# Optimization experiments

Measured on AMD Instinct MI355X. Metric: run time of the kernel, lower is better.

The kernel has to match this reference:

```python
import jax, jax.numpy as jnp
import numpy as np

N, E, F_IN, D, H = 20000, 640000, 128, 16, 8  # nodes, edges, in_features, out_features, n_heads


def _linear_params(k, fan_in, fan_out):
    W = jax.random.normal(k, (fan_in, fan_out), jnp.float32) / np.sqrt(fan_in)
    b = jnp.zeros((fan_out,), jnp.float32)
    return W, b


def setup_inputs() -> dict:
    key = jax.random.key(0)
    ks = jax.random.split(key, 8)
    x = jax.random.normal(ks[0], (N, F_IN), jnp.float32)
    edge_index = jax.random.randint(ks[1], (2, E), 0, N, dtype=jnp.int64)
    Wq, bq = _linear_params(ks[2], F_IN, D * H)
    Wk, bk = _linear_params(ks[3], F_IN, D * H)
    Wv, bv = _linear_params(ks[4], F_IN, D * H)
    Wpsi, bpsi = _linear_params(ks[5], D, D)
    Wo, bo = _linear_params(ks[6], D * H * 2, F_IN)
    gamma = jnp.ones((F_IN,), jnp.float32)
    beta = jnp.zeros((F_IN,), jnp.float32)
    return {"x": x, "edge_index": edge_index, "Wq": Wq, "bq": bq, "Wk": Wk, "bk": bk,
            "Wv": Wv, "bv": bv, "Wpsi": Wpsi, "bpsi": bpsi, "Wo": Wo, "bo": bo,
            "gamma": gamma, "beta": beta}


def _segment_softmax(logits, seg, num_segments):
    # numerically-stable softmax of edge logits grouped by destination node (row)
    m = jax.ops.segment_max(logits, seg, num_segments=num_segments)  # [N,H]
    m = jnp.where(jnp.isfinite(m), m, 0.0)
    e = jnp.exp(logits - m[seg])  # [E,H]
    s = jax.ops.segment_sum(e, seg, num_segments=num_segments)  # [N,H]
    return e / (s[seg] + 1e-16)


def reference(x, edge_index, Wq, bq, Wk, bk, Wv, bv, Wpsi, bpsi, Wo, bo, gamma, beta):
    q = (x @ Wq + bq).reshape(N, H, D)
    k = (x @ Wk + bk).reshape(N, H, D)
    v = (x @ Wv + bv).reshape(N, H, D)
    row, col = edge_index[0], edge_index[1]

    logits = jnp.einsum('ehd,ehd->eh', q[row], k[col]) / np.sqrt(D)  # [E,H]
    alpha = _segment_softmax(logits, row, N)  # [E,H]

    v_j = v[col]  # [E,H,D]
    h_lp = jax.ops.segment_sum((alpha[..., None] * v_j).reshape(E, H * D), row, num_segments=N)
    v_bp = jnp.tanh(v_j @ Wpsi + bpsi)  # per-head linear on last dim, [E,H,D]
    h_bp = jax.ops.segment_sum((alpha[..., None] * v_bp).reshape(E, H * D), row, num_segments=N)

    h_out = jnp.concatenate([h_lp, h_bp], axis=1) @ Wo + bo  # [N,F_IN]
    y = x + jax.nn.relu(h_out)
    mu = jnp.mean(y, axis=-1, keepdims=True)
    var = jnp.mean(jnp.square(y - mu), axis=-1, keepdims=True)
    return (y - mu) * jax.lax.rsqrt(var + 1e-5) * gamma + beta
```

## Files before the change

### kernel.cpp

```cpp
#include <hip/hip_runtime.h>
#include <hip/hip_bf16.h>
#include <math.h>

#define NN 20000
#define EE 640000
#define NCH 8
#define CHN 2500
#define SLOT 24

typedef __attribute__((ext_vector_type(8))) short short8;
typedef __attribute__((ext_vector_type(4))) float f32x4;
typedef __hip_bfloat16 bf16;
typedef __hip_bfloat162 bf162;

__device__ inline ushort f2bf(float f) {
  bf16 h = __float2bfloat16(f);
  return *(ushort*)&h;
}
__device__ inline float2 ldbf2(const ushort* p) {
  return __bfloat1622float2(*(const bf162*)p);
}
__device__ inline float2 bf2u(uint u) {
  return __bfloat1622float2(*(const bf162*)&u);
}
__device__ inline float fast_tanh(float x) {
  float xx = fminf(fmaxf(x, -9.0f), 9.0f);
  float e = exp2f(xx * 2.885390082f);
  return (e - 1.0f) * __builtin_amdgcn_rcpf(e + 1.0f);
}


__global__ __launch_bounds__(256) void qkv_mfma(
    const float* __restrict__ x,
    const float* __restrict__ Wq, const float* __restrict__ bq,
    const float* __restrict__ Wk, const float* __restrict__ bk,
    const float* __restrict__ Wv, const float* __restrict__ bv,
    const float* __restrict__ Wpsi, const float* __restrict__ bpsi,
    float* __restrict__ qbuf, ushort* __restrict__ kvb,
    int* __restrict__ cursor2) {
  __shared__ ushort As[128 * 136];
  __shared__ ushort Bts[128 * 136];
  __shared__ float Wps[256];
  __shared__ float bps[16];
  int t = threadIdx.x;
  {
    int flat = (blockIdx.y * 157 + blockIdx.x) * 256 + t;
    for (int j = flat; j < NN * NCH; j += 157 * 3 * 256) cursor2[j] = 0;
  }
  int n0 = blockIdx.x * 128;
  int mat = blockIdx.y;
  const float* W    = mat == 0 ? Wq : (mat == 1 ? Wk : Wv);
  const float* bias = mat == 0 ? bq : (mat == 1 ? bk : bv);
  if (mat == 2) {
    Wps[t] = Wpsi[t];
    if (t < 16) bps[t] = bpsi[t];
  }

  {
    int r = t >> 1, half = (t & 1) * 64;
    int n = n0 + r;
    ushort* dst = &As[r * 136 + half];
    if (n < NN) {
      const float* src = x + (size_t)n * 128 + half;
#pragma unroll
      for (int j = 0; j < 8; ++j) {
        float4 f0 = *(const float4*)(src + 8 * j);
        float4 f1 = *(const float4*)(src + 8 * j + 4);
        ushort tmp[8] = {f2bf(f0.x), f2bf(f0.y), f2bf(f0.z), f2bf(f0.w),
                         f2bf(f1.x), f2bf(f1.y), f2bf(f1.z), f2bf(f1.w)};
        *(uint4*)(dst + 8 * j) = *(uint4*)tmp;
      }
    } else {
#pragma unroll
      for (int j = 0; j < 8; ++j) *(uint4*)(dst + 8 * j) = make_uint4(0, 0, 0, 0);
    }
  }
  {
    int k = t >> 1, nh = (t & 1) * 64;
    const float* src = W + (size_t)k * 128 + nh;
#pragma unroll
    for (int i = 0; i < 16; ++i) {
      float4 f = *(const float4*)(src + 4 * i);
      Bts[(nh + 4 * i + 0) * 136 + k] = f2bf(f.x);
      Bts[(nh + 4 * i + 1) * 136 + k] = f2bf(f.y);
      Bts[(nh + 4 * i + 2) * 136 + k] = f2bf(f.z);
      Bts[(nh + 4 * i + 3) * 136 + k] = f2bf(f.w);
    }
  }
  __syncthreads();

  int w = t >> 6, lane = t & 63;
  int m = lane & 15, q = lane >> 4;
  int r0 = w * 32;
  f32x4 acc0[8], acc1[8];
#pragma unroll
  for (int c = 0; c < 8; ++c) {
    acc0[c] = (f32x4){0.f, 0.f, 0.f, 0.f};
    acc1[c] = (f32x4){0.f, 0.f, 0.f, 0.f};
  }
#pragma unroll
  for (int kb = 0; kb < 4; ++kb) {
    int kof = kb * 32 + 8 * q;
    short8 a0 = *(const short8*)&As[(r0 + m) * 136 + kof];
    short8 a1 = *(const short8*)&As[(r0 + 16 + m) * 136 + kof];
#pragma unroll
    for (int c = 0; c < 8; ++c) {
      short8 b = *(const short8*)&Bts[(c * 16 + m) * 136 + kof];
      acc0[c] = __builtin_amdgcn_mfma_f32_16x16x32_bf16(a0, b, acc0[c], 0, 0, 0);
      acc1[c] = __builtin_amdgcn_mfma_f32_16x16x32_bf16(a1, b, acc1[c], 0, 0, 0);
    }
  }
  if (mat == 2) __syncthreads();

  int koff2 = (mat == 2) ? 2 : 0;
#pragma unroll
  for (int c = 0; c < 8; ++c) {
    int col = c * 16 + m;
    float bb = bias[col];
    size_t pos = (size_t)(col >> 1) * 6 + (col & 1) + koff2;
#pragma unroll
    for (int reg = 0; reg < 4; ++reg) {
      int rl0 = r0 + 4 * q + reg;
      int rl1 = rl0 + 16;
      int row0 = n0 + rl0;
      int row1 = n0 + rl1;
      float v0 = acc0[c][reg] + bb;
      float v1 = acc1[c][reg] + bb;
      if (mat == 0) {
        if (row0 < NN) qbuf[(size_t)row0 * 128 + col] = v0;
        if (row1 < NN) qbuf[(size_t)row1 * 128 + col] = v1;
      } else {
        if (row0 < NN) kvb[(size_t)row0 * 384 + pos] = f2bf(v0);
        if (row1 < NN) kvb[(size_t)row1 * 384 + pos] = f2bf(v1);
        if (mat == 2) {
          Bts[rl0 * 136 + col] = f2bf(v0);
          Bts[rl1 * 136 + col] = f2bf(v1);
        }
      }
    }
  }

  if (mat == 2) {
    __syncthreads();
#pragma unroll
    for (int ii = 0; ii < 4; ++ii) {
      int idx = ii * 256 + t;
      int rloc = idx >> 3, h = idx & 7;
      int n = n0 + rloc;
      const ushort* vp = &Bts[rloc * 136 + h * 16];
      uint4 a = *(const uint4*)vp;
      uint4 b = *(const uint4*)(vp + 8);
      float v[16];
      {
        float2 f;
        f = bf2u(a.x); v[0] = f.x;  v[1] = f.y;
        f = bf2u(a.y); v[2] = f.x;  v[3] = f.y;
        f = bf2u(a.z); v[4] = f.x;  v[5] = f.y;
        f = bf2u(a.w); v[6] = f.x;  v[7] = f.y;
        f = bf2u(b.x); v[8] = f.x;  v[9] = f.y;
        f = bf2u(b.y); v[10] = f.x; v[11] = f.y;
        f = bf2u(b.z); v[12] = f.x; v[13] = f.y;
        f = bf2u(b.w); v[14] = f.x; v[15] = f.y;
      }
      float o[16];
#pragma unroll
      for (int d = 0; d < 16; ++d) o[d] = bps[d];
#pragma unroll
      for (int dp = 0; dp < 16; ++dp) {
        float vv = v[dp];
#pragma unroll
        for (int d = 0; d < 16; ++d) o[d] = fmaf(vv, Wps[dp * 16 + d], o[d]);
      }
      if (n < NN) {
        ushort* dst = kvb + (size_t)n * 384;
#pragma unroll
        for (int j = 0; j < 8; ++j) {
          uint u = (uint)f2bf(fast_tanh(o[2 * j])) |
                   ((uint)f2bf(fast_tanh(o[2 * j + 1])) << 16);
          *(uint*)(dst + (8 * h + j) * 6 + 4) = u;
        }
      }
    }
  }
}

__global__ __launch_bounds__(256) void scatter_kernel(
    const int* __restrict__ ei,
    int* __restrict__ cursor2, ushort* __restrict__ scol2) {
  int e = blockIdx.x * 256 + threadIdx.x;
  if (e < EE) {
    int r = ei[e];
    int c = ei[EE + e];
    int ch = c / CHN;
    int pos = atomicAdd(&cursor2[r * NCH + ch], 1);
    if (pos < SLOT) scol2[(r * NCH + ch) * SLOT + pos] = (ushort)c;
  }
}

__global__ __launch_bounds__(256) void aggregate_kernel(
    const float* __restrict__ qbuf, const ushort* __restrict__ kvb,
    const int* __restrict__ cursor2, const ushort* __restrict__ scol2,
    ushort* __restrict__ hbufb) {
  int t = threadIdx.x;
  int lane = t & 63;
  int wid = __builtin_amdgcn_readfirstlane(t >> 6);
  int wg = blockIdx.x * 4 + wid;
  int n0 = wg * 4;
  int h = lane >> 3, dg = (lane & 7) * 2;
  int off = h * 16 + dg;
  const float SC = 0.25f * 1.44269504f;

  float q2x[4], q2y[4], s[4], aV0[4], aV1[4], aB0[4], aB1[4];
#pragma unroll
  for (int ni = 0; ni < 4; ++ni) {
    float2 q2 = *(const float2*)(qbuf + (size_t)(n0 + ni) * 128 + off);
    q2x[ni] = q2.x * SC; q2y[ni] = q2.y * SC;
    s[ni] = 0.f; aV0[ni] = 0.f; aV1[ni] = 0.f; aB0[ni] = 0.f; aB1[ni] = 0.f;
  }
  int mycnt = cursor2[n0 * NCH + (lane & 31)];

  const char* kvc = (const char*)kvb;
  uint lo = (uint)lane * 12u;

  for (int ch = 0; ch < NCH; ++ch) {
#pragma unroll
    for (int ni = 0; ni < 4; ++ni) {
      int cnt = __builtin_amdgcn_readfirstlane(__shfl(mycnt, ni * NCH + ch));
      cnt = cnt > SLOT ? SLOT : cnt;
      if (cnt == 0) continue;
      const uint* slu = (const uint*)(scol2 + ((n0 + ni) * NCH + ch) * SLOT);
      float lq2x = q2x[ni], lq2y = q2y[ni];
      float ls = 0.f, lV0 = 0.f, lV1 = 0.f, lB0 = 0.f, lB1 = 0.f;

      struct U3 { uint x, y, z; };
      auto proc = [&](U3 u) {
        float2 kk = bf2u(u.x);
        float2 vv = bf2u(u.y);
        float2 tb = bf2u(u.z);
        float d = fmaf(lq2x, kk.x, lq2y * kk.y);
        d += __shfl_xor(d, 1);
        d += __shfl_xor(d, 2);
        d += __shfl_xor(d, 4);
        float wgt = exp2f(d);
        ls += wgt;
        lV0 = fmaf(wgt, vv.x, lV0); lV1 = fmaf(wgt, vv.y, lV1);
        lB0 = fmaf(wgt, tb.x, lB0); lB1 = fmaf(wgt, tb.y, lB1);
      };

      int i = 0;
      for (; i + 4 <= cnt; i += 4) {
        uint w0 = slu[i >> 1];
        uint w1 = slu[(i >> 1) + 1];
        uint e0 = w0 & 0xffffu, e1 = w0 >> 16, e2 = w1 & 0xffffu, e3 = w1 >> 16;
        const char* p0 = kvc + e0 * 768u;
        const char* p1 = kvc + e1 * 768u;
        const char* p2 = kvc + e2 * 768u;
        const char* p3 = kvc + e3 * 768u;
        U3 u0 = *(const U3*)(p0 + lo);
        U3 u1 = *(const U3*)(p1 + lo);
        U3 u2 = *(const U3*)(p2 + lo);
        U3 u3 = *(const U3*)(p3 + lo);
        proc(u0); proc(u1); proc(u2); proc(u3);
      }
      for (; i < cnt; ++i) {
        uint wv = slu[i >> 1];
        uint e = (i & 1) ? (wv >> 16) : (wv & 0xffffu);
        const char* p = kvc + e * 768u;
        U3 u = *(const U3*)(p + lo);
        proc(u);
      }
      s[ni] += ls;
      aV0[ni] += lV0; aV1[ni] += lV1; aB0[ni] += lB0; aB1[ni] += lB1;
    }
    __syncthreads();
  }

#pragma unroll
  for (int ni = 0; ni < 4; ++ni) {
    float inv = s[ni] > 0.f ? 1.f / s[ni] : 0.f;
    ushort* hp = hbufb + (size_t)(n0 + ni) * 256 + off;
    uint uv = (uint)f2bf(aV0[ni] * inv) | ((uint)f2bf(aV1[ni] * inv) << 16);
    uint ub = (uint)f2bf(aB0[ni] * inv) | ((uint)f2bf(aB1[ni] * inv) << 16);
    *(uint*)(hp)       = uv;
    *(uint*)(hp + 128) = ub;
  }
}

__global__ __launch_bounds__(256) void output_mfma(
    const ushort* __restrict__ hbufb, const float* __restrict__ x,
    const float* __restrict__ Wo, const float* __restrict__ bo,
    const float* __restrict__ gamma, const float* __restrict__ beta,
    float* __restrict__ out) {
  __shared__ ushort As[128 * 136];
  __shared__ ushort Bts[128 * 136];
  __shared__ float bos[128], gs[128], bts[128];
  int t = threadIdx.x;
  int n0 = blockIdx.x * 128;
  if (t < 128) { bos[t] = bo[t]; gs[t] = gamma[t]; bts[t] = beta[t]; }
  int w = t >> 6, lane = t & 63;
  int m = lane & 15, q = lane >> 4;
  int r0 = w * 32;
  f32x4 acc0[8], acc1[8];
#pragma unroll
  for (int c = 0; c < 8; ++c) {
    acc0[c] = (f32x4){0.f, 0.f, 0.f, 0.f};
    acc1[c] = (f32x4){0.f, 0.f, 0.f, 0.f};
  }
  for (int kc = 0; kc < 2; ++kc) {
    if (kc) __syncthreads();
    {
      int r = t >> 1, half = (t & 1) * 64;
      int n = n0 + r;
      ushort* dst = &As[r * 136 + half];
      if (n < NN) {
        const ushort* src = hbufb + (size_t)n * 256 + kc * 128 + half;
#pragma unroll
        for (int j = 0; j < 8; ++j)
          *(uint4*)(dst + 8 * j) = *(const uint4*)(src + 8 * j);
      } else {
#pragma unroll
        for (int j = 0; j < 8; ++j) *(uint4*)(dst + 8 * j) = make_uint4(0, 0, 0, 0);
      }
    }
    {
      int k = t >> 1, nh = (t & 1) * 64;
      const float* src = Wo + (size_t)(kc * 128 + k) * 128 + nh;
#pragma unroll
      for (int i = 0; i < 16; ++i) {
        float4 f = *(const float4*)(src + 4 * i);
        Bts[(nh + 4 * i + 0) * 136 + k] = f2bf(f.x);
        Bts[(nh + 4 * i + 1) * 136 + k] = f2bf(f.y);
        Bts[(nh + 4 * i + 2) * 136 + k] = f2bf(f.z);
        Bts[(nh + 4 * i + 3) * 136 + k] = f2bf(f.w);
      }
    }
    __syncthreads();
#pragma unroll
    for (int kb = 0; kb < 4; ++kb) {
      int kof = kb * 32 + 8 * q;
      short8 a0 = *(const short8*)&As[(r0 + m) * 136 + kof];
      short8 a1 = *(const short8*)&As[(r0 + 16 + m) * 136 + kof];
#pragma unroll
      for (int c = 0; c < 8; ++c) {
        short8 b = *(const short8*)&Bts[(c * 16 + m) * 136 + kof];
        acc0[c] = __builtin_amdgcn_mfma_f32_16x16x32_bf16(a0, b, acc0[c], 0, 0, 0);
        acc1[c] = __builtin_amdgcn_mfma_f32_16x16x32_bf16(a1, b, acc1[c], 0, 0, 0);
      }
    }
  }
#pragma unroll
  for (int half = 0; half < 2; ++half) {
#pragma unroll
    for (int reg = 0; reg < 4; ++reg) {
      int row = n0 + r0 + half * 16 + 4 * q + reg;
      bool valid = row < NN;
      float vals[8];
      float sum = 0.f;
#pragma unroll
      for (int c = 0; c < 8; ++c) {
        int col = c * 16 + m;
        float a = (half ? acc1[c][reg] : acc0[c][reg]) + bos[col];
        a = fmaxf(a, 0.f);
        float xv = valid ? x[(size_t)row * 128 + col] : 0.f;
        float v = a + xv;
        vals[c] = v;
        sum += v;
      }
      sum += __shfl_xor(sum, 1); sum += __shfl_xor(sum, 2);
      sum += __shfl_xor(sum, 4); sum += __shfl_xor(sum, 8);
      float mean = sum * (1.f / 128.f);
      float ssq = 0.f;
#pragma unroll
      for (int c = 0; c < 8; ++c) {
        float d = vals[c] - mean;
        ssq = fmaf(d, d, ssq);
      }
      ssq += __shfl_xor(ssq, 1); ssq += __shfl_xor(ssq, 2);
      ssq += __shfl_xor(ssq, 4); ssq += __shfl_xor(ssq, 8);
      float rstd = rsqrtf(ssq * (1.f / 128.f) + 1e-5f);
      if (valid) {
#pragma unroll
        for (int c = 0; c < 8; ++c) {
          int col = c * 16 + m;
          out[(size_t)row * 128 + col] = (vals[c] - mean) * rstd * gs[col] + bts[col];
        }
      }
    }
  }
}

extern "C" void kernel_launch(void* const* d_in, const int* in_sizes, int n_in,
                              void* d_out, int out_size, void* d_ws, size_t ws_size,
                              hipStream_t stream) {
  const float* x     = (const float*)d_in[0];
  const int*   ei    = (const int*)d_in[1];
  const float* Wq    = (const float*)d_in[2];
  const float* bq    = (const float*)d_in[3];
  const float* Wk    = (const float*)d_in[4];
  const float* bk    = (const float*)d_in[5];
  const float* Wv    = (const float*)d_in[6];
  const float* bv    = (const float*)d_in[7];
  const float* Wpsi  = (const float*)d_in[8];
  const float* bpsi  = (const float*)d_in[9];
  const float* Wo    = (const float*)d_in[10];
  const float* bo    = (const float*)d_in[11];
  const float* gamma = (const float*)d_in[12];
  const float* beta  = (const float*)d_in[13];
  float* out = (float*)d_out;

  char* ws = (char*)d_ws;
  float*  qbuf    = (float*) (ws);
  ushort* kvb     = (ushort*)(ws + 10240000);
  ushort* hbufb   = (ushort*)(ws + 25600000);
  int*    cursor2 = (int*)   (ws + 35840000);
  ushort* scol2   = (ushort*)(ws + 36480000);

  qkv_mfma<<<dim3(157, 3), 256, 0, stream>>>(x, Wq, bq, Wk, bk, Wv, bv,
                                             Wpsi, bpsi, qbuf, kvb, cursor2);
  scatter_kernel<<<2500, 256, 0, stream>>>(ei, cursor2, scol2);
  aggregate_kernel<<<1250, 256, 0, stream>>>(qbuf, kvb, cursor2, scol2, hbufb);
  output_mfma<<<157, 256, 0, stream>>>(hbufb, x, Wo, bo, gamma, beta, out);
}
```

Measured before the change: 227.3 us.

## Regroup K/V/tanh layout into 4-element chunks and process two edges per wave

```diff
diff --git a/kernel.cpp b/kernel.cpp
--- a/kernel.cpp
+++ b/kernel.cpp
@@ -112,12 +112,12 @@
   }
   if (mat == 2) __syncthreads();
 
-  int koff2 = (mat == 2) ? 2 : 0;
+  int koff2 = (mat == 2) ? 4 : 0;
 #pragma unroll
   for (int c = 0; c < 8; ++c) {
     int col = c * 16 + m;
     float bb = bias[col];
-    size_t pos = (size_t)(col >> 1) * 6 + (col & 1) + koff2;
+    size_t pos = (size_t)(c * 4 + (m >> 2)) * 12 + (m & 3) + koff2;
 #pragma unroll
     for (int reg = 0; reg < 4; ++reg) {
       int rl0 = r0 + 4 * q + reg;
@@ -177,7 +177,9 @@
         for (int j = 0; j < 8; ++j) {
           uint u = (uint)f2bf(fast_tanh(o[2 * j])) |
                    ((uint)f2bf(fast_tanh(o[2 * j + 1])) << 16);
-          *(uint*)(dst + (8 * h + j) * 6 + 4) = u;
+          int grp = h * 4 + (j >> 1);
+          int within = (2 * j) & 3;
+          *(uint*)(dst + grp * 12 + 8 + within) = u;
         }
       }
     }
@@ -205,84 +207,95 @@
   int lane = t & 63;
   int wid = __builtin_amdgcn_readfirstlane(t >> 6);
   int wg = blockIdx.x * 4 + wid;
-  int n0 = wg * 4;
-  int h = lane >> 3, dg = (lane & 7) * 2;
-  int off = h * 16 + dg;
+  int n0 = wg * 2;
+  int l31 = lane & 31;
+  int half = lane >> 5;
   const float SC = 0.25f * 1.44269504f;
 
-  float q2x[4], q2y[4], s[4], aV0[4], aV1[4], aB0[4], aB1[4];
-#pragma unroll
-  for (int ni = 0; ni < 4; ++ni) {
-    float2 q2 = *(const float2*)(qbuf + (size_t)(n0 + ni) * 128 + off);
-    q2x[ni] = q2.x * SC; q2y[ni] = q2.y * SC;
-    s[ni] = 0.f; aV0[ni] = 0.f; aV1[ni] = 0.f; aB0[ni] = 0.f; aB1[ni] = 0.f;
-  }
-  int mycnt = cursor2[n0 * NCH + (lane & 31)];
+  float4 q0 = *(const float4*)(qbuf + (size_t)n0 * 128 + l31 * 4);
+  float4 q1 = *(const float4*)(qbuf + (size_t)(n0 + 1) * 128 + l31 * 4);
+  q0.x *= SC; q0.y *= SC; q0.z *= SC; q0.w *= SC;
+  q1.x *= SC; q1.y *= SC; q1.z *= SC; q1.w *= SC;
+
+  int mycnt = cursor2[n0 * NCH + (lane & 15)];
+
+  float s0 = 0.f, s1 = 0.f;
+  float4 aV0 = make_float4(0.f, 0.f, 0.f, 0.f), aV1 = aV0;
+  float4 aB0 = aV0, aB1 = aV0;
 
   const char* kvc = (const char*)kvb;
-  uint lo = (uint)lane * 12u;
+  uint lo24 = (uint)l31 * 24u;
 
   for (int ch = 0; ch < NCH; ++ch) {
 #pragma unroll
-    for (int ni = 0; ni < 4; ++ni) {
+    for (int ni = 0; ni < 2; ++ni) {
       int cnt = __builtin_amdgcn_readfirstlane(__shfl(mycnt, ni * NCH + ch));
       cnt = cnt > SLOT ? SLOT : cnt;
       if (cnt == 0) continue;
       const uint* slu = (const uint*)(scol2 + ((n0 + ni) * NCH + ch) * SLOT);
-      float lq2x = q2x[ni], lq2y = q2y[ni];
-      float ls = 0.f, lV0 = 0.f, lV1 = 0.f, lB0 = 0.f, lB1 = 0.f;
-
-      struct U3 { uint x, y, z; };
-      auto proc = [&](U3 u) {
-        float2 kk = bf2u(u.x);
-        float2 vv = bf2u(u.y);
-        float2 tb = bf2u(u.z);
-        float d = fmaf(lq2x, kk.x, lq2y * kk.y);
+      float4 q = ni ? q1 : q0;
+      float ls = 0.f;
+      float4 lV = make_float4(0.f, 0.f, 0.f, 0.f);
+      float4 lB = make_float4(0.f, 0.f, 0.f, 0.f);
+      int npair = (cnt + 1) >> 1;
+      for (int p = 0; p < npair; ++p) {
+        uint wv = slu[p];
+        uint e0 = wv & 0xffffu;
+        uint e1 = wv >> 16;
+        bool pv = (2 * p + 1) < cnt;
+        uint e1c = pv ? e1 : e0;
+        uint e = half ? e1c : e0;
+        const char* pb = kvc + (size_t)e * 768u + lo24;
+        uint4 L0 = *(const uint4*)pb;
+        uint2 L1 = *(const uint2*)(pb + 16);
+        float2 k0 = bf2u(L0.x), k1 = bf2u(L0.y);
+        float d = fmaf(q.x, k0.x, fmaf(q.y, k0.y, fmaf(q.z, k1.x, q.w * k1.y)));
         d += __shfl_xor(d, 1);
         d += __shfl_xor(d, 2);
-        d += __shfl_xor(d, 4);
         float wgt = exp2f(d);
+        wgt = (half && !pv) ? 0.f : wgt;
         ls += wgt;
-        lV0 = fmaf(wgt, vv.x, lV0); lV1 = fmaf(wgt, vv.y, lV1);
-        lB0 = fmaf(wgt, tb.x, lB0); lB1 = fmaf(wgt, tb.y, lB1);
-      };
-
-      int i = 0;
-      for (; i + 4 <= cnt; i += 4) {
-        uint w0 = slu[i >> 1];
-        uint w1 = slu[(i >> 1) + 1];
-        uint e0 = w0 & 0xffffu, e1 = w0 >> 16, e2 = w1 & 0xffffu, e3 = w1 >> 16;
-        const char* p0 = kvc + e0 * 768u;
-        const char* p1 = kvc + e1 * 768u;
-        const char* p2 = kvc + e2 * 768u;
-        const char* p3 = kvc + e3 * 768u;
-        U3 u0 = *(const U3*)(p0 + lo);
-        U3 u1 = *(const U3*)(p1 + lo);
-        U3 u2 = *(const U3*)(p2 + lo);
-        U3 u3 = *(const U3*)(p3 + lo);
-        proc(u0); proc(u1); proc(u2); proc(u3);
-      }
-      for (; i < cnt; ++i) {
-        uint wv = slu[i >> 1];
-        uint e = (i & 1) ? (wv >> 16) : (wv & 0xffffu);
-        const char* p = kvc + e * 768u;
-        U3 u = *(const U3*)(p + lo);
-        proc(u);
-      }
-      s[ni] += ls;
-      aV0[ni] += lV0; aV1[ni] += lV1; aB0[ni] += lB0; aB1[ni] += lB1;
+        float2 v0 = bf2u(L0.z), v1 = bf2u(L0.w);
+        lV.x = fmaf(wgt, v0.x, lV.x); lV.y = fmaf(wgt, v0.y, lV.y);
+        lV.z = fmaf(wgt, v1.x, lV.z); lV.w = fmaf(wgt, v1.y, lV.w);
+        float2 b0 = bf2u(L1.x), b1 = bf2u(L1.y);
+        lB.x = fmaf(wgt, b0.x, lB.x); lB.y = fmaf(wgt, b0.y, lB.y);
+        lB.z = fmaf(wgt, b1.x, lB.z); lB.w = fmaf(wgt, b1.y, lB.w);
+      }
+      if (ni == 0) {
+        s0 += ls;
+        aV0.x += lV.x; aV0.y += lV.y; aV0.z += lV.z; aV0.w += lV.w;
+        aB0.x += lB.x; aB0.y += lB.y; aB0.z += lB.z; aB0.w += lB.w;
+      } else {
+        s1 += ls;
+        aV1.x += lV.x; aV1.y += lV.y; aV1.z += lV.z; aV1.w += lV.w;
+        aB1.x += lB.x; aB1.y += lB.y; aB1.z += lB.z; aB1.w += lB.w;
+      }
     }
     __syncthreads();
   }
 
 #pragma unroll
-  for (int ni = 0; ni < 4; ++ni) {
-    float inv = s[ni] > 0.f ? 1.f / s[ni] : 0.f;
-    ushort* hp = hbufb + (size_t)(n0 + ni) * 256 + off;
-    uint uv = (uint)f2bf(aV0[ni] * inv) | ((uint)f2bf(aV1[ni] * inv) << 16);
-    uint ub = (uint)f2bf(aB0[ni] * inv) | ((uint)f2bf(aB1[ni] * inv) << 16);
-    *(uint*)(hp)       = uv;
-    *(uint*)(hp + 128) = ub;
+  for (int ni = 0; ni < 2; ++ni) {
+    float s = ni ? s1 : s0;
+    float4 V = ni ? aV1 : aV0;
+    float4 B = ni ? aB1 : aB0;
+    s += __shfl_xor(s, 32);
+    V.x += __shfl_xor(V.x, 32); V.y += __shfl_xor(V.y, 32);
+    V.z += __shfl_xor(V.z, 32); V.w += __shfl_xor(V.w, 32);
+    B.x += __shfl_xor(B.x, 32); B.y += __shfl_xor(B.y, 32);
+    B.z += __shfl_xor(B.z, 32); B.w += __shfl_xor(B.w, 32);
+    float inv = s > 0.f ? 1.f / s : 0.f;
+    if (half == 0) {
+      ushort* hp = hbufb + (size_t)(n0 + ni) * 256 + l31 * 4;
+      uint2 uv, ub;
+      uv.x = (uint)f2bf(V.x * inv) | ((uint)f2bf(V.y * inv) << 16);
+      uv.y = (uint)f2bf(V.z * inv) | ((uint)f2bf(V.w * inv) << 16);
+      ub.x = (uint)f2bf(B.x * inv) | ((uint)f2bf(B.y * inv) << 16);
+      ub.y = (uint)f2bf(B.z * inv) | ((uint)f2bf(B.w * inv) << 16);
+      *(uint2*)(hp)       = uv;
+      *(uint2*)(hp + 128) = ub;
+    }
   }
 }
 
@@ -418,6 +431,6 @@
   qkv_mfma<<<dim3(157, 3), 256, 0, stream>>>(x, Wq, bq, Wk, bk, Wv, bv,
                                              Wpsi, bpsi, qbuf, kvb, cursor2);
   scatter_kernel<<<2500, 256, 0, stream>>>(ei, cursor2, scol2);
-  aggregate_kernel<<<1250, 256, 0, stream>>>(qbuf, kvb, cursor2, scol2, hbufb);
+  aggregate_kernel<<<2500, 256, 0, stream>>>(qbuf, kvb, cursor2, scol2, hbufb);
   output_mfma<<<157, 256, 0, stream>>>(hbufb, x, Wo, bo, gamma, beta, out);
 }
```

After: 233.8 us. 2.8% more time.

## Fuse edge scatter into QKV kernel and simplify aggregation to per-node CSR rows

Applied to the files above, without the earlier changes.

```diff
diff --git a/kernel.cpp b/kernel.cpp
--- a/kernel.cpp
+++ b/kernel.cpp
@@ -4,9 +4,6 @@
 
 #define NN 20000
 #define EE 640000
-#define NCH 8
-#define CHN 2500
-#define SLOT 24
 
 typedef __attribute__((ext_vector_type(8))) short short8;
 typedef __attribute__((ext_vector_type(4))) float f32x4;
@@ -16,9 +13,6 @@
 __device__ inline ushort f2bf(float f) {
   bf16 h = __float2bfloat16(f);
   return *(ushort*)&h;
-}
-__device__ inline float2 ldbf2(const ushort* p) {
-  return __bfloat1622float2(*(const bf162*)p);
 }
 __device__ inline float2 bf2u(uint u) {
   return __bfloat1622float2(*(const bf162*)&u);
@@ -36,19 +30,28 @@
     const float* __restrict__ Wk, const float* __restrict__ bk,
     const float* __restrict__ Wv, const float* __restrict__ bv,
     const float* __restrict__ Wpsi, const float* __restrict__ bpsi,
-    float* __restrict__ qbuf, ushort* __restrict__ kvb,
-    int* __restrict__ cursor2) {
+    const int* __restrict__ ei,
+    float* __restrict__ qbuf,
+    ushort* __restrict__ kb, ushort* __restrict__ vb2, ushort* __restrict__ bb2,
+    int* __restrict__ cursor, ushort* __restrict__ scol) {
   __shared__ ushort As[128 * 136];
-  __shared__ ushort Bts[128 * 136];
+  __shared__ ushort WB[128 * 136];
   __shared__ float Wps[256];
   __shared__ float bps[16];
   int t = threadIdx.x;
+  int mat = blockIdx.y;
+
   {
-    int flat = (blockIdx.y * 157 + blockIdx.x) * 256 + t;
-    for (int j = flat; j < NN * NCH; j += 157 * 3 * 256) cursor2[j] = 0;
-  }
+    int flat = (mat * 157 + blockIdx.x) * 256 + t;
+    for (int e = flat; e < EE; e += 157 * 3 * 256) {
+      int r = ei[e];
+      int c = ei[EE + e];
+      int pos = atomicAdd(&cursor[r], 1);
+      if (pos < 128) scol[r * 128 + pos] = (ushort)c;
+    }
+  }
+
   int n0 = blockIdx.x * 128;
-  int mat = blockIdx.y;
   const float* W    = mat == 0 ? Wq : (mat == 1 ? Wk : Wv);
   const float* bias = mat == 0 ? bq : (mat == 1 ? bk : bv);
   if (mat == 2) {
@@ -81,10 +84,10 @@
 #pragma unroll
     for (int i = 0; i < 16; ++i) {
       float4 f = *(const float4*)(src + 4 * i);
-      Bts[(nh + 4 * i + 0) * 136 + k] = f2bf(f.x);
-      Bts[(nh + 4 * i + 1) * 136 + k] = f2bf(f.y);
-      Bts[(nh + 4 * i + 2) * 136 + k] = f2bf(f.z);
-      Bts[(nh + 4 * i + 3) * 136 + k] = f2bf(f.w);
+      WB[(nh + 4 * i + 0) * 136 + k] = f2bf(f.x);
+      WB[(nh + 4 * i + 1) * 136 + k] = f2bf(f.y);
+      WB[(nh + 4 * i + 2) * 136 + k] = f2bf(f.z);
+      WB[(nh + 4 * i + 3) * 136 + k] = f2bf(f.w);
     }
   }
   __syncthreads();
@@ -99,55 +102,54 @@
     acc1[c] = (f32x4){0.f, 0.f, 0.f, 0.f};
   }
 #pragma unroll
-  for (int kb = 0; kb < 4; ++kb) {
-    int kof = kb * 32 + 8 * q;
+  for (int kb_ = 0; kb_ < 4; ++kb_) {
+    int kof = kb_ * 32 + 8 * q;
     short8 a0 = *(const short8*)&As[(r0 + m) * 136 + kof];
     short8 a1 = *(const short8*)&As[(r0 + 16 + m) * 136 + kof];
 #pragma unroll
     for (int c = 0; c < 8; ++c) {
-      short8 b = *(const short8*)&Bts[(c * 16 + m) * 136 + kof];
+      short8 b = *(const short8*)&WB[(c * 16 + m) * 136 + kof];
       acc0[c] = __builtin_amdgcn_mfma_f32_16x16x32_bf16(a0, b, acc0[c], 0, 0, 0);
       acc1[c] = __builtin_amdgcn_mfma_f32_16x16x32_bf16(a1, b, acc1[c], 0, 0, 0);
     }
   }
-  if (mat == 2) __syncthreads();
-
-  int koff2 = (mat == 2) ? 2 : 0;
+
+  if (mat == 0) {
+#pragma unroll
+    for (int c = 0; c < 8; ++c) {
+      int col = c * 16 + m;
+      float bb = bias[col];
+#pragma unroll
+      for (int reg = 0; reg < 4; ++reg) {
+        int row0 = n0 + r0 + 4 * q + reg;
+        int row1 = row0 + 16;
+        if (row0 < NN) qbuf[(size_t)row0 * 128 + col] = acc0[c][reg] + bb;
+        if (row1 < NN) qbuf[(size_t)row1 * 128 + col] = acc1[c][reg] + bb;
+      }
+    }
+    return;
+  }
+
+  __syncthreads();
 #pragma unroll
   for (int c = 0; c < 8; ++c) {
     int col = c * 16 + m;
     float bb = bias[col];
-    size_t pos = (size_t)(col >> 1) * 6 + (col & 1) + koff2;
 #pragma unroll
     for (int reg = 0; reg < 4; ++reg) {
       int rl0 = r0 + 4 * q + reg;
-      int rl1 = rl0 + 16;
-      int row0 = n0 + rl0;
-      int row1 = n0 + rl1;
-      float v0 = acc0[c][reg] + bb;
-      float v1 = acc1[c][reg] + bb;
-      if (mat == 0) {
-        if (row0 < NN) qbuf[(size_t)row0 * 128 + col] = v0;
-        if (row1 < NN) qbuf[(size_t)row1 * 128 + col] = v1;
-      } else {
-        if (row0 < NN) kvb[(size_t)row0 * 384 + pos] = f2bf(v0);
-        if (row1 < NN) kvb[(size_t)row1 * 384 + pos] = f2bf(v1);
-        if (mat == 2) {
-          Bts[rl0 * 136 + col] = f2bf(v0);
-          Bts[rl1 * 136 + col] = f2bf(v1);
-        }
-      }
-    }
-  }
+      As[rl0 * 136 + col]        = f2bf(acc0[c][reg] + bb);
+      As[(rl0 + 16) * 136 + col] = f2bf(acc1[c][reg] + bb);
+    }
+  }
+  __syncthreads();
 
   if (mat == 2) {
-    __syncthreads();
 #pragma unroll
     for (int ii = 0; ii < 4; ++ii) {
-      int idx = ii * 256 + t;
-      int rloc = idx >> 3, h = idx & 7;
-      int n = n0 + rloc;
-      const ushort* vp = &Bts[rloc * 136 + h * 16];
+      int cell = ii * 256 + t;
+      int rl = cell >> 3, h = cell & 7;
+      const ushort* vp = &As[rl * 136 + h * 16];
       uint4 a = *(const uint4*)vp;
       uint4 b = *(const uint4*)(vp + 8);
       float v[16];
@@ -171,119 +173,100 @@
 #pragma unroll
         for (int d = 0; d < 16; ++d) o[d] = fmaf(vv, Wps[dp * 16 + d], o[d]);
       }
-      if (n < NN) {
-        ushort* dst = kvb + (size_t)n * 384;
-#pragma unroll
-        for (int j = 0; j < 8; ++j) {
-          uint u = (uint)f2bf(fast_tanh(o[2 * j])) |
-                   ((uint)f2bf(fast_tanh(o[2 * j + 1])) << 16);
-          *(uint*)(dst + (8 * h + j) * 6 + 4) = u;
-        }
-      }
-    }
-  }
-}
-
-__global__ __launch_bounds__(256) void scatter_kernel(
-    const int* __restrict__ ei,
-    int* __restrict__ cursor2, ushort* __restrict__ scol2) {
-  int e = blockIdx.x * 256 + threadIdx.x;
-  if (e < EE) {
-    int r = ei[e];
-    int c = ei[EE + e];
-    int ch = c / CHN;
-    int pos = atomicAdd(&cursor2[r * NCH + ch], 1);
-    if (pos < SLOT) scol2[(r * NCH + ch) * SLOT + pos] = (ushort)c;
+      ushort* dst = &WB[rl * 136 + h * 16];
+#pragma unroll
+      for (int j = 0; j < 8; ++j) {
+        uint u = (uint)f2bf(fast_tanh(o[2 * j])) |
+                 ((uint)f2bf(fast_tanh(o[2 * j + 1])) << 16);
+        *(uint*)(dst + 2 * j) = u;
+      }
+    }
+    __syncthreads();
+  }
+
+  {
+    int r = t >> 1, hh = (t & 1) * 64;
+    int n = n0 + r;
+    if (n < NN) {
+      ushort* dstA = (mat == 1 ? kb : vb2) + (size_t)n * 128 + hh;
+      const ushort* srcA = &As[r * 136 + hh];
+#pragma unroll
+      for (int j = 0; j < 8; ++j)
+        *(uint4*)(dstA + 8 * j) = *(const uint4*)(srcA + 8 * j);
+      if (mat == 2) {
+        ushort* dstB = bb2 + (size_t)n * 128 + hh;
+        const ushort* srcB = &WB[r * 136 + hh];
+#pragma unroll
+        for (int j = 0; j < 8; ++j)
+          *(uint4*)(dstB + 8 * j) = *(const uint4*)(srcB + 8 * j);
+      }
+    }
   }
 }
 
 __global__ __launch_bounds__(256) void aggregate_kernel(
-    const float* __restrict__ qbuf, const ushort* __restrict__ kvb,
-    const int* __restrict__ cursor2, const ushort* __restrict__ scol2,
+    const float* __restrict__ qbuf,
+    const ushort* __restrict__ kb, const ushort* __restrict__ vb2,
+    const ushort* __restrict__ bb2,
+    const int* __restrict__ cursor, const ushort* __restrict__ scol,
     ushort* __restrict__ hbufb) {
-  int t = threadIdx.x;
-  int lane = t & 63;
-  int wid = __builtin_amdgcn_readfirstlane(t >> 6);
-  int wg = blockIdx.x * 4 + wid;
-  int n0 = wg * 4;
+  int wid = threadIdx.x >> 6, lane = threadIdx.x & 63;
+  int node = blockIdx.x * 4 + wid;
   int h = lane >> 3, dg = (lane & 7) * 2;
   int off = h * 16 + dg;
   const float SC = 0.25f * 1.44269504f;
-
-  float q2x[4], q2y[4], s[4], aV0[4], aV1[4], aB0[4], aB1[4];
-#pragma unroll
-  for (int ni = 0; ni < 4; ++ni) {
-    float2 q2 = *(const float2*)(qbuf + (size_t)(n0 + ni) * 128 + off);
-    q2x[ni] = q2.x * SC; q2y[ni] = q2.y * SC;
-    s[ni] = 0.f; aV0[ni] = 0.f; aV1[ni] = 0.f; aB0[ni] = 0.f; aB1[ni] = 0.f;
-  }
-  int mycnt = cursor2[n0 * NCH + (lane & 31)];
-
-  const char* kvc = (const char*)kvb;
-  uint lo = (uint)lane * 12u;
-
-  for (int ch = 0; ch < NCH; ++ch) {
-#pragma unroll
-    for (int ni = 0; ni < 4; ++ni) {
-      int cnt = __builtin_amdgcn_readfirstlane(__shfl(mycnt, ni * NCH + ch));
-      cnt = cnt > SLOT ? SLOT : cnt;
-      if (cnt == 0) continue;
-      const uint* slu = (const uint*)(scol2 + ((n0 + ni) * NCH + ch) * SLOT);
-      float lq2x = q2x[ni], lq2y = q2y[ni];
-      float ls = 0.f, lV0 = 0.f, lV1 = 0.f, lB0 = 0.f, lB1 = 0.f;
-
-      struct U3 { uint x, y, z; };
-      auto proc = [&](U3 u) {
-        float2 kk = bf2u(u.x);
-        float2 vv = bf2u(u.y);
-        float2 tb = bf2u(u.z);
-        float d = fmaf(lq2x, kk.x, lq2y * kk.y);
-        d += __shfl_xor(d, 1);
-        d += __shfl_xor(d, 2);
-        d += __shfl_xor(d, 4);
-        float wgt = exp2f(d);
-        ls += wgt;
-        lV0 = fmaf(wgt, vv.x, lV0); lV1 = fmaf(wgt, vv.y, lV1);
-        lB0 = fmaf(wgt, tb.x, lB0); lB1 = fmaf(wgt, tb.y, lB1);
-      };
-
-      int i = 0;
-      for (; i + 4 <= cnt; i += 4) {
-        uint w0 = slu[i >> 1];
-        uint w1 = slu[(i >> 1) + 1];
-        uint e0 = w0 & 0xffffu, e1 = w0 >> 16, e2 = w1 & 0xffffu, e3 = w1 >> 16;
-        const char* p0 = kvc + e0 * 768u;
-        const char* p1 = kvc + e1 * 768u;
-        const char* p2 = kvc + e2 * 768u;
-        const char* p3 = kvc + e3 * 768u;
-        U3 u0 = *(const U3*)(p0 + lo);
-        U3 u1 = *(const U3*)(p1 + lo);
-        U3 u2 = *(const U3*)(p2 + lo);
-        U3 u3 = *(const U3*)(p3 + lo);
-        proc(u0); proc(u1); proc(u2); proc(u3);
-      }
-      for (; i < cnt; ++i) {
-        uint wv = slu[i >> 1];
-        uint e = (i & 1) ? (wv >> 16) : (wv & 0xffffu);
-        const char* p = kvc + e * 768u;
-        U3 u = *(const U3*)(p + lo);
-        proc(u);
-      }
-      s[ni] += ls;
-      aV0[ni] += lV0; aV1[ni] += lV1; aB0[ni] += lB0; aB1[ni] += lB1;
-    }
-    __syncthreads();
-  }
-
-#pragma unroll
-  for (int ni = 0; ni < 4; ++ni) {
-    float inv = s[ni] > 0.f ? 1.f / s[ni] : 0.f;
-    ushort* hp = hbufb + (size_t)(n0 + ni) * 256 + off;
-    uint uv = (uint)f2bf(aV0[ni] * inv) | ((uint)f2bf(aV1[ni] * inv) << 16);
-    uint ub = (uint)f2bf(aB0[ni] * inv) | ((uint)f2bf(aB1[ni] * inv) << 16);
-    *(uint*)(hp)       = uv;
-    *(uint*)(hp + 128) = ub;
-  }
+  float2 q2 = *(const float2*)(qbuf + (size_t)node * 128 + off);
+  q2.x *= SC; q2.y *= SC;
+  int cnt = cursor[node];
+  cnt = cnt > 128 ? 128 : cnt;
+  const ushort* srow = scol + node * 128;
+  float s = 0.f, aV0 = 0.f, aV1 = 0.f, aB0 = 0.f, aB1 = 0.f;
+
+  auto proc1 = [&](uint K, uint V, uint B) {
+    float2 kk = bf2u(K);
+    float d = fmaf(q2.x, kk.x, q2.y * kk.y);
+    d += __shfl_xor(d, 1);
+    d += __shfl_xor(d, 2);
+    d += __shfl_xor(d, 4);
+    float wgt = exp2f(d);
+    s += wgt;
+    float2 vv = bf2u(V);
+    aV0 = fmaf(wgt, vv.x, aV0); aV1 = fmaf(wgt, vv.y, aV1);
+    float2 tb = bf2u(B);
+    aB0 = fmaf(wgt, tb.x, aB0); aB1 = fmaf(wgt, tb.y, aB1);
+  };
+
+  int i = 0;
+  for (; i + 8 <= cnt; i += 8) {
+    uint4 wv = *(const uint4*)(srow + i);
+    int id[8] = {(int)(wv.x & 0xffffu), (int)(wv.x >> 16),
+                 (int)(wv.y & 0xffffu), (int)(wv.y >> 16),
+                 (int)(wv.z & 0xffffu), (int)(wv.z >> 16),
+                 (int)(wv.w & 0xffffu), (int)(wv.w >> 16)};
+    uint K[8], V[8], B[8];
+#pragma unroll
+    for (int j = 0; j < 8; ++j) {
+      size_t base = (size_t)id[j] * 128 + off;
+      K[j] = *(const uint*)(kb + base);
+      V[j] = *(const uint*)(vb2 + base);
+      B[j] = *(const uint*)(bb2 + base);
+    }
+#pragma unroll
+    for (int j = 0; j < 8; ++j) proc1(K[j], V[j], B[j]);
+  }
+  for (; i < cnt; ++i) {
+    int e = srow[i];
+    size_t base = (size_t)e * 128 + off;
+    proc1(*(const uint*)(kb + base), *(const uint*)(vb2 + base),
+          *(const uint*)(bb2 + base));
+  }
+
+  float inv = s > 0.f ? 1.f / s : 0.f;
+  ushort* hp = hbufb + (size_t)node * 256 + off;
+  uint uv = (uint)f2bf(aV0 * inv) | ((uint)f2bf(aV1 * inv) << 16);
+  uint ub = (uint)f2bf(aB0 * inv) | ((uint)f2bf(aB1 * inv) << 16);
+  *(uint*)(hp)       = uv;
+  *(uint*)(hp + 128) = ub;
 }
 
 __global__ __launch_bounds__(256) void output_mfma(
@@ -409,15 +392,20 @@
   float* out = (float*)d_out;
 
   char* ws = (char*)d_ws;
-  float*  qbuf    = (float*) (ws);
-  ushort* kvb     = (ushort*)(ws + 10240000);
-  ushort* hbufb   = (ushort*)(ws + 25600000);
-  int*    cursor2 = (int*)   (ws + 35840000);
-  ushort* scol2   = (ushort*)(ws + 36480000);
+  float*  qbuf   = (float*) (ws);
+  ushort* kb     = (ushort*)(ws + 10240000);
+  ushort* vb2    = (ushort*)(ws + 15360000);
+  ushort* bb2    = (ushort*)(ws + 20480000);
+  ushort* hbufb  = (ushort*)(ws + 25600000);
+  int*    cursor = (int*)   (ws + 35840000);
+  ushort* scol   = (ushort*)(ws + 35920000);
+
+  hipMemsetAsync(cursor, 0, 80000, stream);
 
   qkv_mfma<<<dim3(157, 3), 256, 0, stream>>>(x, Wq, bq, Wk, bk, Wv, bv,
-                                             Wpsi, bpsi, qbuf, kvb, cursor2);
-  scatter_kernel<<<2500, 256, 0, stream>>>(ei, cursor2, scol2);
-  aggregate_kernel<<<1250, 256, 0, stream>>>(qbuf, kvb, cursor2, scol2, hbufb);
+                                             Wpsi, bpsi, ei, qbuf,
+                                             kb, vb2, bb2, cursor, scol);
+  aggregate_kernel<<<5000, 256, 0, stream>>>(qbuf, kb, vb2, bb2, cursor, scol,
+                                             hbufb);
   output_mfma<<<157, 256, 0, stream>>>(hbufb, x, Wo, bo, gamma, beta, out);
 }
```

Measured after the change: 285.0 us. +25.4%, slower.
